# Performance work log

Hardware: AMD Instinct MI355X
Metric: run time of the kernel (lower is better)

Reference implementation:

```python
import jax, jax.numpy as jnp
import numpy as np

IN_F, H1, H2, NC = 784, 1024, 1024, 10
BATCH = 32
EPS = 0.1


def setup_inputs() -> dict:
    key = jax.random.key(0)
    ks = jax.random.split(key, 8)
    x = jax.random.normal(ks[0], (BATCH, IN_F), jnp.float32)
    y = jax.random.randint(ks[1], (BATCH,), 0, NC)
    W1 = jax.random.normal(ks[2], (H1, IN_F), jnp.float32) / np.float32(np.sqrt(IN_F))
    b1 = jax.random.normal(ks[3], (H1,), jnp.float32) * 0.01
    W2 = jax.random.normal(ks[4], (H2, H1), jnp.float32) / np.float32(np.sqrt(H1))
    b2 = jax.random.normal(ks[5], (H2,), jnp.float32) * 0.01
    W3 = jax.random.normal(ks[6], (NC, H2), jnp.float32) / np.float32(np.sqrt(H2))
    b3 = jax.random.normal(ks[7], (NC,), jnp.float32) * 0.01
    return dict(x=x, y=y, W1=W1, b1=b1, W2=W2, b2=b2, W3=W3, b3=b3)


def _relu_coeffs(zl, zu):
    # d = 1 where zl>=0, zu/(zu-zl) where crossing, 0 where zu<=0 (as in select_layer)
    I = (zl < 0) & (zu > 0)
    d = jnp.where(zl >= 0, 1.0, jnp.where(I, zu / (zu - zl), 0.0))
    lI = jnp.where(I, zl, 0.0)  # zl restricted to crossing set I
    return d, lI


def reference(x, y, W1, b1, W2, b2, W3, b3):
    eps = jnp.float32(EPS)
    # ---- layer-1 preactivation bounds (InfBall fval) ----
    nom1 = x @ W1.T + b1                              # [B,H1]
    r1 = eps * jnp.abs(W1).sum(1)                     # [H1]
    zl1, zu1 = nom1 - r1, nom1 + r1
    d1, l1m = _relu_coeffs(zl1, zu1)                  # [B,H1]

    # ---- layer-2 preactivation bounds via dual (transpose) propagation, nu = I ----
    nu1 = W2[None, :, :] * d1[:, None, :]             # [B,H2,H1]  (D1 W2^T rows)
    V0 = jnp.einsum('bji,ik->bjk', nu1, W1)           # [B,H2,IN]
    A = jnp.einsum('bjk,bk->bj', V0, x) + b2 + nu1 @ b1
    E = eps * jnp.abs(V0).sum(-1)
    crossl = jnp.einsum('bji,bi->bj', jax.nn.relu(-nu1), l1m)
    crossu = jnp.einsum('bji,bi->bj', jax.nn.relu(nu1), l1m)
    zl2 = A - E + crossl
    zu2 = A + E - crossu
    d2, l2m = _relu_coeffs(zl2, zu2)                  # [B,H2]

    # ---- final robust bounds: c[b,j,:] = e_{y_b} - e_j ----
    eye = jnp.eye(NC, dtype=x.dtype)
    c = eye[y][:, None, :] - eye[None, :, :]          # [B,NC,NC]
    nu2 = (c @ W3) * d2[:, None, :]                   # [B,NC,H2]
    nu1f = (nu2 @ W2) * d1[:, None, :]                # [B,NC,H1]
    V0f = nu1f @ W1                                   # [B,NC,IN]
    Af = jnp.einsum('bjk,bk->bj', V0f, x) + c @ b3 + nu2 @ b2 + nu1f @ b1
    Ef = eps * jnp.abs(V0f).sum(-1)
    crossf = (jnp.einsum('bji,bi->bj', jax.nn.relu(-nu2), l2m)
              + jnp.einsum('bji,bi->bj', jax.nn.relu(-nu1f), l1m))
    J = Af - Ef + crossf                              # lower bound of c^T z
    return -J                                         # f: upper bound of z_j - z_y, [B,NC]
```

## Files before the change

kernel.cpp:

```cpp
#include <hip/hip_runtime.h>
#include <math.h>

#define B    32
#define INF  784
#define H1   1024
#define H2   1024
#define NC   10
#define EPSV 0.1f

typedef __attribute__((ext_vector_type(8))) short short8;
typedef __attribute__((ext_vector_type(4))) float floatx4;

__device__ inline ushort bf16_rne(float f) {
  uint u = __builtin_bit_cast(uint, f);
  u += 0x7FFFu + ((u >> 16) & 1u);
  return (ushort)(u >> 16);
}
__device__ inline uint pack2(float a, float b) {
  return (uint)bf16_rne(a) | ((uint)bf16_rne(b) << 16);
}
__device__ inline uint scale_pack(uint u, float d0, float d1v) {
  float f0 = __builtin_bit_cast(float, u << 16) * d0;
  float f1 = __builtin_bit_cast(float, u & 0xFFFF0000u) * d1v;
  uint r0 = __builtin_bit_cast(uint, f0) + 0x8000u;
  uint r1 = __builtin_bit_cast(uint, f1) + 0x8000u;
  return __builtin_amdgcn_perm(r1, r0, 0x07060302u);
}

__global__ __launch_bounds__(256) void k_pre(
    const float* __restrict__ x, const float* __restrict__ W1,
    const float* __restrict__ b1, const float* __restrict__ W2,
    ushort* __restrict__ W1F, ushort* __restrict__ W2F,
    float* __restrict__ d1B, float* __restrict__ t1B, float* __restrict__ dnB,
    float* __restrict__ Ezero)
{
  __shared__ float red[4][B + 1];
  __shared__ float Ts[4][32][17];
  int bid = blockIdx.x;
  int t = threadIdx.x;
  if (bid < 64) {
    int jt = bid;
    int lane = t & 63, c0 = t >> 6;
    int l15 = lane & 15, quad = lane >> 4;
    for (int c = c0; c < 32; c += 4) {
      const float* src = &W2[(size_t)(jt * 16 + l15) * H1 + c * 32 + quad * 8];
      float4 v0 = *reinterpret_cast<const float4*>(src);
      float4 v1 = *reinterpret_cast<const float4*>(src + 4);
      uint4 o;
      o.x = pack2(v0.x, v0.y); o.y = pack2(v0.z, v0.w);
      o.z = pack2(v1.x, v1.y); o.w = pack2(v1.z, v1.w);
      *reinterpret_cast<uint4*>(&W2F[((size_t)(c * 64 + jt) * 64 + lane) * 8]) = o;
    }
  } else if (bid < 113) {
    int mt = bid - 64;
    int col0 = mt * 16;
    int w = t >> 6, lane = t & 63;
    int l15 = lane & 15, quad = lane >> 4;
    for (int cg = 0; cg < 8; cg++) {
      int c = cg * 4 + w;
#pragma unroll
      for (int p = 0; p < 8; p++) {
        int r = p * 4 + (lane >> 4);
        Ts[w][r][lane & 15] = W1[(size_t)(c * 32 + r) * INF + col0 + (lane & 15)];
      }
      float f[8];
#pragma unroll
      for (int e = 0; e < 8; e++) f[e] = Ts[w][quad * 8 + e][l15];
      uint4 o;
      o.x = pack2(f[0], f[1]); o.y = pack2(f[2], f[3]);
      o.z = pack2(f[4], f[5]); o.w = pack2(f[6], f[7]);
      *reinterpret_cast<uint4*>(&W1F[((size_t)(c * 49 + mt) * 64 + lane) * 8]) = o;
    }
  } else if (bid < 1137) {
    int i = bid - 113;
    const float* w = W1 + (size_t)i * INF;
    float acc[B];
#pragma unroll
    for (int b = 0; b < B; b++) acc[b] = 0.f;
    float wabs = 0.f;
    for (int k = t; k < INF; k += 256) {
      float wv = w[k];
      wabs += fabsf(wv);
#pragma unroll
      for (int b = 0; b < B; b++) acc[b] = fmaf(x[b * INF + k], wv, acc[b]);
    }
#pragma unroll
    for (int off = 32; off > 0; off >>= 1) {
#pragma unroll
      for (int b = 0; b < B; b++) acc[b] += __shfl_down(acc[b], off, 64);
      wabs += __shfl_down(wabs, off, 64);
    }
    int wave = t >> 6, lane = t & 63;
    if (lane == 0) {
#pragma unroll
      for (int b = 0; b < B; b++) red[wave][b] = acc[b];
      red[wave][B] = wabs;
    }
    __syncthreads();
    if (t < B) {
      float s = red[0][t] + red[1][t] + red[2][t] + red[3][t];
      float r = EPSV * (red[0][B] + red[1][B] + red[2][B] + red[3][B]);
      float nom = s + b1[i];
      float zl = nom - r, zu = nom + r;
      float d, l;
      if (zl >= 0.f)      { d = 1.f;            l = 0.f; }
      else if (zu > 0.f)  { d = zu / (zu - zl); l = zl;  }
      else                { d = 0.f;            l = 0.f; }
      d1B[(size_t)t * H1 + i] = d;
      t1B[(size_t)t * H1 + i] = d * l;
      dnB[(size_t)t * H1 + i] = d * nom;
    }
  } else {
    int zb = bid - 1137;
    for (int idx = t; idx < 8192; idx += 256) {
      int pos = zb * 8192 + idx;
      if (pos < 54272) Ezero[pos] = 0.f;
    }
  }
}

__global__ __launch_bounds__(256) void k3s(
    const ushort* __restrict__ W2F, const float* __restrict__ d1B,
    ushort* __restrict__ W2D)
{
  int bid = blockIdx.x;
  int xcd = bid & 7, q = bid >> 3;
  int c = xcd * 4 + (q >> 5);
  int b = q & 31;
  int t = threadIdx.x, w = t >> 6, lane = t & 63;
  int quad = lane >> 4;
  __shared__ float ds[32];
  if (t < 32) ds[t] = d1B[(size_t)b * H1 + c * 32 + t];
  __syncthreads();
  float4 dv0 = *reinterpret_cast<const float4*>(&ds[quad * 8]);
  float4 dv1 = *reinterpret_cast<const float4*>(&ds[quad * 8 + 4]);
  const ushort* src = W2F + ((size_t)(c * 64) * 64 + lane) * 8;
  ushort* dst = W2D + (size_t)b * 1048576 + ((size_t)(c * 64) * 64 + lane) * 8;
  for (int jt = w; jt < 64; jt += 4) {
    uint4 u = *reinterpret_cast<const uint4*>(src + (size_t)jt * 512);
    uint4 o;
    o.x = scale_pack(u.x, dv0.x, dv0.y);
    o.y = scale_pack(u.y, dv0.z, dv0.w);
    o.z = scale_pack(u.z, dv1.x, dv1.y);
    o.w = scale_pack(u.w, dv1.z, dv1.w);
    *reinterpret_cast<uint4*>(dst + (size_t)jt * 512) = o;
  }
}

#define K3D_LOAD(c, A, B0, B1) do {                                             \
  _Pragma("unroll")                                                             \
  for (int ni = 0; ni < 2; ni++) {                                              \
    B0[ni] = *reinterpret_cast<const uint4*>(bBase0 + (size_t)(c) * 32768 + ni * 512); \
    B1[ni] = *reinterpret_cast<const uint4*>(bBase1 + (size_t)(c) * 32768 + ni * 512); \
  }                                                                             \
  _Pragma("unroll")                                                             \
  for (int mi = 0; mi < 7; mi++)                                                \
    A[mi] = *reinterpret_cast<const uint4*>(aBase + (size_t)(c) * 25088 + mi * 512); \
} while (0)

#define K3D_COMP(A, Bv, accB) do {                                              \
  _Pragma("unroll")                                                             \
  for (int mi = 0; mi < 7; mi++) {                                              \
    short8 af = __builtin_bit_cast(short8, A[mi]);                              \
    _Pragma("unroll")                                                           \
    for (int ni = 0; ni < 2; ni++)                                              \
      accB[mi][ni] = __builtin_amdgcn_mfma_f32_16x16x32_bf16(af, __builtin_bit_cast(short8, Bv[ni]), accB[mi][ni], 0, 0, 0); \
  }                                                                             \
} while (0)

__global__ __launch_bounds__(256, 2) void k3d(
    const ushort* __restrict__ W1F, const ushort* __restrict__ W2D,
    float* __restrict__ E)
{
  int bid = blockIdx.x;
  int xcd = bid & 7, q = bid >> 3;
  int x = q % 7;
  int yz = xcd * 16 + q / 7;
  int by = yz & 7, bz = yz >> 3;
  int b0 = bz * 2;
  int t = threadIdx.x, w = t >> 6, lane = t & 63;
  int l15 = lane & 15;
  int mt0 = x * 7;
  int jt0 = by * 8 + w * 2;

  const ushort* aBase = W1F + ((size_t)mt0 * 64 + lane) * 8;
  const ushort* bBase0 = W2D + (size_t)b0 * 1048576 + ((size_t)jt0 * 64 + lane) * 8;
  const ushort* bBase1 = bBase0 + 1048576;

  floatx4 acc[2][7][2];
#pragma unroll
  for (int bb = 0; bb < 2; bb++)
#pragma unroll
    for (int mi = 0; mi < 7; mi++)
#pragma unroll
      for (int ni = 0; ni < 2; ni++) acc[bb][mi][ni] = (floatx4){0.f, 0.f, 0.f, 0.f};

  uint4 a0[7], a1[7], p00[2], p01[2], p10[2], p11[2];
  K3D_LOAD(0, a0, p00, p01);
  K3D_LOAD(1, a1, p10, p11);
  for (int c = 0; c < 30; c += 2) {
    K3D_COMP(a0, p00, acc[0]);
    K3D_COMP(a0, p01, acc[1]);
    K3D_LOAD(c + 2, a0, p00, p01);
    K3D_COMP(a1, p10, acc[0]);
    K3D_COMP(a1, p11, acc[1]);
    if (c + 3 < 32) K3D_LOAD(c + 3, a1, p10, p11);
  }
  K3D_COMP(a0, p00, acc[0]);
  K3D_COMP(a0, p01, acc[1]);
  K3D_COMP(a1, p10, acc[0]);
  K3D_COMP(a1, p11, acc[1]);

#pragma unroll
  for (int bb = 0; bb < 2; bb++) {
#pragma unroll
    for (int ni = 0; ni < 2; ni++) {
      float s = 0.f;
#pragma unroll
      for (int mi = 0; mi < 7; mi++)
#pragma unroll
        for (int r = 0; r < 4; r++) s += fabsf(acc[bb][mi][ni][r]);
      s += __shfl_xor(s, 16, 64);
      s += __shfl_xor(s, 32, 64);
      if (lane < 16) {
        int j = (jt0 + ni) * 16 + l15;
        atomicAdd(&E[(size_t)j * B + b0 + bb], EPSV * s);
      }
    }
  }
}

#define K3_LOAD(c, A, Bv) do {                                                  \
  _Pragma("unroll")                                                             \
  for (int ni = 0; ni < 2; ni++)                                                \
    Bv[ni] = *reinterpret_cast<const uint4*>(bBase + (size_t)(c) * 32768 + ni * 512); \
  _Pragma("unroll")                                                             \
  for (int mi = 0; mi < 7; mi++)                                                \
    A[mi] = *reinterpret_cast<const uint4*>(aBase + (size_t)(c) * 25088 + mi * 512); \
} while (0)

#define K3F_COMP(c, A, Bv, DsRow, accB) do {                                    \
  float4 dv0 = *reinterpret_cast<const float4*>(&DsRow[(c) * 32]);              \
  float4 dv1 = *reinterpret_cast<const float4*>(&DsRow[(c) * 32 + 4]);          \
  short8 bfr[2];                                                                \
  _Pragma("unroll")                                                             \
  for (int ni = 0; ni < 2; ni++) {                                              \
    uint4 sb;                                                                   \
    sb.x = scale_pack(Bv[ni].x, dv0.x, dv0.y);                                  \
    sb.y = scale_pack(Bv[ni].y, dv0.z, dv0.w);                                  \
    sb.z = scale_pack(Bv[ni].z, dv1.x, dv1.y);                                  \
    sb.w = scale_pack(Bv[ni].w, dv1.z, dv1.w);                                  \
    bfr[ni] = __builtin_bit_cast(short8, sb);                                   \
  }                                                                             \
  _Pragma("unroll")                                                             \
  for (int mi = 0; mi < 7; mi++) {                                              \
    short8 af = __builtin_bit_cast(short8, A[mi]);                              \
    _Pragma("unroll")                                                           \
    for (int ni = 0; ni < 2; ni++)                                              \
      accB[mi][ni] = __builtin_amdgcn_mfma_f32_16x16x32_bf16(af, bfr[ni], accB[mi][ni], 0, 0, 0); \
  }                                                                             \
} while (0)

__global__ __launch_bounds__(256, 2) void k3(
    const ushort* __restrict__ W1F, const ushort* __restrict__ W2F,
    const float* __restrict__ d1B, float* __restrict__ E)
{
  int b0 = blockIdx.z * 2;
  int t = threadIdx.x, w = t >> 6, lane = t & 63;
  int quad = lane >> 4, l15 = lane & 15;
  int mt0 = blockIdx.x * 7;
  int jt0 = blockIdx.y * 8 + w * 2;

  __shared__ float Ds[2][H1];
  for (int idx = t; idx < 2 * H1; idx += 256)
    Ds[idx >> 10][idx & 1023] = d1B[(size_t)(b0 + (idx >> 10)) * H1 + (idx & 1023)];
  __syncthreads();

  const ushort* aBase = W1F + ((size_t)mt0 * 64 + lane) * 8;
  const ushort* bBase = W2F + ((size_t)jt0 * 64 + lane) * 8;
  const float* Ds0 = &Ds[0][quad * 8];
  const float* Ds1 = &Ds[1][quad * 8];

  floatx4 acc[2][7][2];
#pragma unroll
  for (int bb = 0; bb < 2; bb++)
#pragma unroll
    for (int mi = 0; mi < 7; mi++)
#pragma unroll
      for (int ni = 0; ni < 2; ni++) acc[bb][mi][ni] = (floatx4){0.f, 0.f, 0.f, 0.f};

  uint4 a0[7], b0v[2], a1[7], b1v[2];
  K3_LOAD(0, a0, b0v);
  K3_LOAD(1, a1, b1v);
  for (int c = 0; c < 30; c += 2) {
    K3F_COMP(c, a0, b0v, Ds0, acc[0]);
    K3F_COMP(c, a0, b0v, Ds1, acc[1]);
    K3_LOAD(c + 2, a0, b0v);
    K3F_COMP(c + 1, a1, b1v, Ds0, acc[0]);
    K3F_COMP(c + 1, a1, b1v, Ds1, acc[1]);
    if (c + 3 < 32) K3_LOAD(c + 3, a1, b1v);
  }
  K3F_COMP(30, a0, b0v, Ds0, acc[0]);
  K3F_COMP(30, a0, b0v, Ds1, acc[1]);
  K3F_COMP(31, a1, b1v, Ds0, acc[0]);
  K3F_COMP(31, a1, b1v, Ds1, acc[1]);

#pragma unroll
  for (int bb = 0; bb < 2; bb++) {
#pragma unroll
    for (int ni = 0; ni < 2; ni++) {
      float s = 0.f;
#pragma unroll
      for (int mi = 0; mi < 7; mi++)
#pragma unroll
        for (int r = 0; r < 4; r++) s += fabsf(acc[bb][mi][ni][r]);
      s += __shfl_xor(s, 16, 64);
      s += __shfl_xor(s, 32, 64);
      if (lane < 16) {
        int j = (jt0 + ni) * 16 + l15;
        atomicAdd(&E[(size_t)j * B + b0 + bb], EPSV * s);
      }
    }
  }
}

__global__ __launch_bounds__(256) void k245a(
    const float* __restrict__ W2, const float* __restrict__ b2,
    const float* __restrict__ dnB, const float* __restrict__ t1B,
    const float* __restrict__ E, const float* __restrict__ W3,
    const int* __restrict__ y,
    float* __restrict__ nu2T, float* __restrict__ F2)
{
  int j = blockIdx.x;
  int t = threadIdx.x;
  int wave = t >> 6, lane = t & 63;
  int b0 = wave * 8;
  float aA[8] = {}, aCl[8] = {}, aCu[8] = {};
  const float* __restrict__ w2 = W2 + (size_t)j * H1;
  for (int i = lane; i < H1; i += 64) {
    float wv = w2[i];
    float wp = fmaxf(wv, 0.f), wn = fmaxf(-wv, 0.f);
#pragma unroll
    for (int r = 0; r < 8; r++) {
      float dv = dnB[(size_t)(b0 + r) * H1 + i];
      float tv = t1B[(size_t)(b0 + r) * H1 + i];
      aA[r]  = fmaf(wv, dv, aA[r]);
      aCl[r] = fmaf(wn, tv, aCl[r]);
      aCu[r] = fmaf(wp, tv, aCu[r]);
    }
  }
#pragma unroll
  for (int off = 32; off > 0; off >>= 1) {
#pragma unroll
    for (int r = 0; r < 8; r++) {
      aA[r]  += __shfl_down(aA[r],  off, 64);
      aCl[r] += __shfl_down(aCl[r], off, 64);
      aCu[r] += __shfl_down(aCu[r], off, 64);
    }
  }
  __shared__ float sA[B], sCl[B], sCu[B];
  __shared__ float sd2[B], st2[B], sdb[B], swy[B], sw3[NC];
  float bj = b2[j];
  if (lane == 0) {
#pragma unroll
    for (int r = 0; r < 8; r++) {
      sA [b0 + r] = aA[r] + bj;
      sCl[b0 + r] = aCl[r];
      sCu[b0 + r] = aCu[r];
    }
  }
  if (t >= 64 && t < 96)   swy[t - 64]  = W3[(size_t)y[t - 64] * H2 + j];
  if (t >= 128 && t < 138) sw3[t - 128] = W3[(size_t)(t - 128) * H2 + j];
  __syncthreads();
  if (t < B) {
    float a = sA[t], e = E[(size_t)j * B + t];
    float zl = a - e + sCl[t];
    float zu = a + e - sCu[t];
    float d, l;
    if (zl >= 0.f)      { d = 1.f;            l = 0.f; }
    else if (zu > 0.f)  { d = zu / (zu - zl); l = zl;  }
    else                { d = 0.f;            l = 0.f; }
    sd2[t] = d;
    st2[t] = d * l;
    sdb[t] = d * bj;
  }
  __syncthreads();
  for (int tt = t; tt < B * NC; tt += 256) {
    int b = tt / NC, jc = tt - b * NC;
    float cw = swy[b] - sw3[jc];
    float d2v = sd2[b];
    nu2T[((size_t)b * H2 + j) * 12 + jc] = cw * d2v;
    float val = cw * sdb[b] + fmaxf(-cw, 0.f) * st2[b];
    atomicAdd(&F2[((size_t)(j & 63) * B + b) * NC + jc], val);
  }
}

__global__ __launch_bounds__(256) void k5b1(
    const float* __restrict__ W2, const float* __restrict__ nu2T,
    float* __restrict__ hpart)
{
  int t = threadIdx.x;
  int i1 = blockIdx.x * 512 + t * 2;
  int b = blockIdx.y, s = blockIdx.z;
  const float* __restrict__ nrowb = nu2T + ((size_t)b * H2 + s * 128) * 12;
  const float* __restrict__ w2b = W2 + (size_t)s * 128 * H1 + i1;
  float h0[NC] = {}, h1[NC] = {};
  for (int i2 = 0; i2 < 128; i2++) {
    float2 wv = *reinterpret_cast<const float2*>(&w2b[(size_t)i2 * H1]);
    const float* __restrict__ nrow = nrowb + i2 * 12;
#pragma unroll
    for (int j = 0; j < NC; j++) {
      h0[j] = fmaf(nrow[j], wv.x, h0[j]);
      h1[j] = fmaf(nrow[j], wv.y, h1[j]);
    }
  }
#pragma unroll
  for (int j = 0; j < NC; j++) {
    float2 o; o.x = h0[j]; o.y = h1[j];
    *reinterpret_cast<float2*>(&hpart[(((size_t)s * B + b) * NC + j) * H1 + i1]) = o;
  }
}

__global__ __launch_bounds__(256) void k5b2(
    const float* __restrict__ hpart,
    const float* __restrict__ d1B, const float* __restrict__ t1B,
    const float* __restrict__ dnB,
    float* __restrict__ nu1fT, float* __restrict__ F)
{
  int t = threadIdx.x;
  int i1 = blockIdx.x * 256 + t;
  int b = blockIdx.y;
  float d1v = d1B[(size_t)b * H1 + i1];
  float t1v = t1B[(size_t)b * H1 + i1];
  float dnv = dnB[(size_t)b * H1 + i1];
  float sn[NC], c1[NC];
#pragma unroll
  for (int j = 0; j < NC; j++) {
    float hv = 0.f;
#pragma unroll
    for (int s = 0; s < 8; s++)
      hv += hpart[(((size_t)s * B + b) * NC + j) * H1 + i1];
    nu1fT[((size_t)b * H1 + i1) * 12 + j] = hv * d1v;
    sn[j] = hv * dnv;
    c1[j] = fmaxf(-hv, 0.f) * t1v;
  }
#pragma unroll
  for (int off = 32; off > 0; off >>= 1) {
#pragma unroll
    for (int j = 0; j < NC; j++) {
      sn[j] += __shfl_down(sn[j], off, 64);
      c1[j] += __shfl_down(c1[j], off, 64);
    }
  }
  __shared__ float red[4][2 * NC];
  int wave = t >> 6, lane = t & 63;
  if (lane == 0) {
#pragma unroll
    for (int j = 0; j < NC; j++) { red[wave][j] = sn[j]; red[wave][NC + j] = c1[j]; }
  }
  __syncthreads();
  if (t < NC) {
    float s = 0.f;
    for (int w = 0; w < 4; w++) s += red[w][t] + red[w][NC + t];
    atomicAdd(&F[b * NC + t], s);
  }
}

__global__ __launch_bounds__(128) void k5c1(
    const float* __restrict__ W1, const float* __restrict__ nu1fT,
    float* __restrict__ ppart)
{
  int t = threadIdx.x;
  bool valid = (t < 112);
  int k = blockIdx.x * 112 + (valid ? t : 0);
  int b = blockIdx.y, s = blockIdx.z;
  const float* __restrict__ nrowb = nu1fT + ((size_t)b * H1 + s * 128) * 12;
  const float* __restrict__ w1b = W1 + (size_t)s * 128 * INF + k;
  float acc[NC] = {};
  for (int i1 = 0; i1 < 128; i1++) {
    float w1v = w1b[(size_t)i1 * INF];
    const float* __restrict__ nrow = nrowb + i1 * 12;
#pragma unroll
    for (int j = 0; j < NC; j++) acc[j] = fmaf(nrow[j], w1v, acc[j]);
  }
  if (valid) {
#pragma unroll
    for (int j = 0; j < NC; j++)
      ppart[(((size_t)s * B + b) * NC + j) * INF + k] = acc[j];
  }
}

__global__ __launch_bounds__(256) void k5c2_out(
    const float* __restrict__ ppart, const float* __restrict__ F,
    const float* __restrict__ F2, const float* __restrict__ b3,
    const int* __restrict__ y, float* __restrict__ out)
{
  int b = blockIdx.x;
  int t = threadIdx.x;
  float e[NC] = {};
  for (int k = t; k < INF; k += 256) {
#pragma unroll
    for (int j = 0; j < NC; j++) {
      float v = 0.f;
#pragma unroll
      for (int s = 0; s < 8; s++)
        v += ppart[(((size_t)s * B + b) * NC + j) * INF + k];
      e[j] += fabsf(v);
    }
  }
#pragma unroll
  for (int off = 32; off > 0; off >>= 1) {
#pragma unroll
    for (int j = 0; j < NC; j++) e[j] += __shfl_down(e[j], off, 64);
  }
  __shared__ float red[4][NC];
  int wave = t >> 6, lane = t & 63;
  if (lane == 0) {
#pragma unroll
    for (int j = 0; j < NC; j++) red[wave][j] = e[j];
  }
  __syncthreads();
  if (t < NC) {
    float ef = 0.f;
    for (int w = 0; w < 4; w++) ef += red[w][t];
    float s = F[b * NC + t];
    for (int slot = 0; slot < 64; slot++)
      s += F2[((size_t)slot * B + b) * NC + t];
    int yb = y[b];
    s += b3[yb] - b3[t];
    out[b * NC + t] = EPSV * ef - s;
  }
}

extern "C" void kernel_launch(void* const* d_in, const int* in_sizes, int n_in,
                              void* d_out, int out_size, void* d_ws, size_t ws_size,
                              hipStream_t stream) {
  const float* x  = (const float*)d_in[0];
  const int*   y  = (const int*)  d_in[1];
  const float* W1 = (const float*)d_in[2];
  const float* b1 = (const float*)d_in[3];
  const float* W2 = (const float*)d_in[4];
  const float* b2 = (const float*)d_in[5];
  const float* W3 = (const float*)d_in[6];
  const float* b3 = (const float*)d_in[7];
  float* out = (float*)d_out;
  float* ws  = (float*)d_ws;

  float* d1B  = ws;
  float* t1B  = ws + 32768;
  float* dnB  = ws + 65536;
  float* E    = ws + 196608;
  float* F    = ws + 229376;
  float* F2   = ws + 230400;
  float* nu2T = ws + 328704;
  ushort* W2F = (ushort*)(ws + 721920);
  ushort* W1F = (ushort*)(ws + 1246208);
  float* nu1fT = ws + 328704;
  float* hpart = ws + 721920;
  float* ppart = ws + 721920;
  const size_t W2D_OFF = 1648640;
  ushort* W2D = (ushort*)(ws + W2D_OFF);
  const size_t WS_NEED = (W2D_OFF + 16777216) * sizeof(float);

  k_pre<<<1144, 256, 0, stream>>>(x, W1, b1, W2, W1F, W2F, d1B, t1B, dnB, E);
  if (ws_size >= WS_NEED) {
    k3s<<<1024, 256, 0, stream>>>(W2F, d1B, W2D);
    k3d<<<896, 256, 0, stream>>>(W1F, W2D, E);
  } else {
    k3<<<dim3(7, 8, 16), 256, 0, stream>>>(W1F, W2F, d1B, E);
  }
  k245a<<<H2, 256, 0, stream>>>(W2, b2, dnB, t1B, E, W3, y, nu2T, F2);
  k5b1<<<dim3(2, B, 8), 256, 0, stream>>>(W2, nu2T, hpart);
  k5b2<<<dim3(4, B), 256, 0, stream>>>(hpart, d1B, t1B, dnB, nu1fT, F);
  k5c1<<<dim3(7, B, 8), 128, 0, stream>>>(W1, nu1fT, ppart);
  k5c2_out<<<B, 256, 0, stream>>>(ppart, F, F2, b3, y, out);
}
```

Baseline: 223.0 us.

## Split scaled-W2 materialization and GEMM into two half-batch passes

The per-batch D1-scaled W2 buffer (32 x 1024x1024 bf16, 64 MB) is now built and consumed in two halves of 16 batches, reusing a 32 MB workspace. The block-to-XCD mapping is changed so each XCD handles two batches, letting the k3d blocks on that XCD read the W2D slices that k3s on the same XCD just wrote. The goal is to keep the intermediate resident in the last-level cache instead of going through HBM. The cost is two extra kernel launches and lower parallelism per launch (448 GEMM blocks instead of 896).

```diff
diff --git a/kernel.cpp b/kernel.cpp
--- a/kernel.cpp
+++ b/kernel.cpp
@@ -121,12 +121,13 @@
 
 __global__ __launch_bounds__(256) void k3s(
     const ushort* __restrict__ W2F, const float* __restrict__ d1B,
-    ushort* __restrict__ W2D)
+    ushort* __restrict__ W2Dh, int bbase)
 {
   int bid = blockIdx.x;
   int xcd = bid & 7, q = bid >> 3;
-  int c = xcd * 4 + (q >> 5);
-  int b = q & 31;
+  int bl = 2 * xcd + (q & 1);
+  int c  = q >> 1;
+  int b  = bbase + bl;
   int t = threadIdx.x, w = t >> 6, lane = t & 63;
   int quad = lane >> 4;
   __shared__ float ds[32];
@@ -134,8 +135,8 @@
   __syncthreads();
   float4 dv0 = *reinterpret_cast<const float4*>(&ds[quad * 8]);
   float4 dv1 = *reinterpret_cast<const float4*>(&ds[quad * 8 + 4]);
-  const ushort* src = W2F + ((size_t)(c * 64) * 64 + lane) * 8;
-  ushort* dst = W2D + (size_t)b * 1048576 + ((size_t)(c * 64) * 64 + lane) * 8;
+  const ushort* src = W2F + (size_t)c * 32768 + lane * 8;
+  ushort* dst = W2Dh + (size_t)bl * 1048576 + (size_t)c * 32768 + lane * 8;
   for (int jt = w; jt < 64; jt += 4) {
     uint4 u = *reinterpret_cast<const uint4*>(src + (size_t)jt * 512);
     uint4 o;
@@ -169,22 +170,21 @@
 } while (0)
 
 __global__ __launch_bounds__(256, 2) void k3d(
-    const ushort* __restrict__ W1F, const ushort* __restrict__ W2D,
-    float* __restrict__ E)
+    const ushort* __restrict__ W1F, const ushort* __restrict__ W2Dh,
+    float* __restrict__ E, int bbase)
 {
   int bid = blockIdx.x;
   int xcd = bid & 7, q = bid >> 3;
-  int x = q % 7;
-  int yz = xcd * 16 + q / 7;
-  int by = yz & 7, bz = yz >> 3;
-  int b0 = bz * 2;
+  int x = q % 7, by = q / 7;
+  int bl0 = 2 * xcd;
+  int b0 = bbase + bl0;
   int t = threadIdx.x, w = t >> 6, lane = t & 63;
   int l15 = lane & 15;
   int mt0 = x * 7;
   int jt0 = by * 8 + w * 2;
 
   const ushort* aBase = W1F + ((size_t)mt0 * 64 + lane) * 8;
-  const ushort* bBase0 = W2D + (size_t)b0 * 1048576 + ((size_t)jt0 * 64 + lane) * 8;
+  const ushort* bBase0 = W2Dh + (size_t)bl0 * 1048576 + ((size_t)jt0 * 64 + lane) * 8;
   const ushort* bBase1 = bBase0 + 1048576;
 
   floatx4 acc[2][7][2];
@@ -559,13 +559,15 @@
   float* hpart = ws + 721920;
   float* ppart = ws + 721920;
   const size_t W2D_OFF = 1648640;
-  ushort* W2D = (ushort*)(ws + W2D_OFF);
-  const size_t WS_NEED = (W2D_OFF + 16777216) * sizeof(float);
+  ushort* W2Dh = (ushort*)(ws + W2D_OFF);
+  const size_t WS_NEED = (W2D_OFF + 8388608) * sizeof(float);
 
   k_pre<<<1144, 256, 0, stream>>>(x, W1, b1, W2, W1F, W2F, d1B, t1B, dnB, E);
   if (ws_size >= WS_NEED) {
-    k3s<<<1024, 256, 0, stream>>>(W2F, d1B, W2D);
-    k3d<<<896, 256, 0, stream>>>(W1F, W2D, E);
+    k3s<<<512, 256, 0, stream>>>(W2F, d1B, W2Dh, 0);
+    k3d<<<448, 256, 0, stream>>>(W1F, W2Dh, E, 0);
+    k3s<<<512, 256, 0, stream>>>(W2F, d1B, W2Dh, 16);
+    k3d<<<448, 256, 0, stream>>>(W1F, W2Dh, E, 16);
   } else {
     k3<<<dim3(7, 8, 16), 256, 0, stream>>>(W1F, W2F, d1B, E);
   }
```

After: 236.3 us. +5.9%, slower.
